# Kernel tuning notes

Measured on AMD Instinct MI355X. Metric: run time of the kernel, lower is better.

Reference implementation:

```python
import jax, jax.numpy as jnp
import numpy as np

CODEBOOK_SIZE = 4096
EMBED_DIM = 256
BETA = 0.25


def setup_inputs() -> dict:
    key = jax.random.key(0)
    k_z, k_cb = jax.random.split(key)
    z = jax.random.normal(k_z, (32, 256, 32, 32), dtype=jnp.float32)
    # nn.Embedding weight init: uniform(-1/D, 1/D)
    codebook = jax.random.uniform(
        k_cb, (CODEBOOK_SIZE, EMBED_DIM), dtype=jnp.float32,
        minval=-1.0 / EMBED_DIM, maxval=1.0 / EMBED_DIM)
    return {"z": z, "codebook": codebook}


def reference(z, codebook):
    b, c, h, w = z.shape
    # (B,C,H,W) -> (B*H*W, D)
    z_flat = jnp.transpose(z, (0, 2, 3, 1)).reshape(-1, c)
    # squared euclidean distances: ||z||^2 - 2 z.e^T + ||e||^2  (== cdist(...)^2)
    z_sq = jnp.sum(z_flat * z_flat, axis=1, keepdims=True)          # (N,1)
    e_sq = jnp.sum(codebook * codebook, axis=1)                     # (K,)
    distances = z_sq - 2.0 * (z_flat @ codebook.T) + e_sq[None, :]  # (N,K)
    min_encoding_indices = jnp.argmin(distances, axis=1)            # (N,)
    z_q_flat = codebook[min_encoding_indices]                       # (N,D)
    z_q = jnp.transpose(z_q_flat.reshape(b, h, w, c), (0, 3, 1, 2))  # (B,C,H,W)
    # straight-through estimator
    z_q_st = z + jax.lax.stop_gradient(z_q - z)
    codebook_loss = jnp.mean((z_q - jax.lax.stop_gradient(z)) ** 2)
    commitment_loss = jnp.mean((z - jax.lax.stop_gradient(z_q)) ** 2)
    vq_loss = codebook_loss + BETA * commitment_loss
    return (z_q_st, vq_loss, min_encoding_indices.reshape(b, h, w))
```

## Files before the change

kernel.cpp:

```cpp
#include <hip/hip_runtime.h>

#define K_CODES 4096
#define D 256
#define N_VEC 32768
#define N_ELEM 8388608
#define WINDOW 3.5e-4f
#define RG 8
#define RSLICE 256

typedef _Float16 f16x8 __attribute__((ext_vector_type(8)));
typedef float f32x4 __attribute__((ext_vector_type(4)));

#define WS_LOSS 0
#define WS_COUNT 8
#define WS_DONE 16
#define WS_IDX 256
#define WS_LIST (WS_IDX + N_VEC * 4)
#define WS_ESQ (WS_LIST + N_VEC * 4)
#define WS_ZSQ (WS_ESQ + K_CODES * 4)
#define WS_APACK (WS_ZSQ + N_VEC * 4)
#define WS_BPACK (WS_APACK + (size_t)N_VEC * 256 * 2)
#define WS_RFIN (WS_BPACK + (size_t)K_CODES * 256 * 2 + 65536)
#define WS_ZT (WS_RFIN + (size_t)N_VEC * 8)
#define WS_NEED_ZT (WS_ZT + (size_t)N_VEC * D * 4)

#define PREP_PZ 4096
#define PREP_PCB 512
#define PREP_ESQ 1024
#define PREP_ZSQ 128
#define PREP_BLOCKS (PREP_PZ + PREP_PCB + PREP_ESQ + PREP_ZSQ)

__device__ __forceinline__ unsigned long long pack_key(float s, int idx) {
  const unsigned u = __float_as_uint(s);
  const unsigned mk = (u & 0x80000000u) ? ~u : (u | 0x80000000u);
  return ((unsigned long long)mk << 12) | (unsigned long long)(unsigned)idx;
}
__device__ __forceinline__ float key_score(unsigned long long k) {
  const unsigned mk = (unsigned)(k >> 12);
  const unsigned u = (mk & 0x80000000u) ? (mk & 0x7fffffffu) : ~mk;
  return __uint_as_float(u);
}

__device__ __forceinline__ void pin_frag(f16x8& v) {
  asm volatile("" : "+v"(v));
}

__device__ void esq_body(int bx, const float* __restrict__ cb,
                         float* __restrict__ esq) {
  const int lane = threadIdx.x & 63;
  const int k = bx * 4 + (threadIdx.x >> 6);
  const float* row = cb + (size_t)k * D;
  double s = 0.;
#pragma unroll
  for (int j = 0; j < 4; ++j) {
    const float v = row[lane + 64 * j];
    s += (double)__fmul_rn(v, v);
  }
#pragma unroll
  for (int off = 32; off > 0; off >>= 1) s += __shfl_down(s, off, 64);
  if (lane == 0) esq[k] = (float)s;
}

__device__ void zsq_body(int bx, const float* __restrict__ z,
                         float* __restrict__ zsq) {
  const int n = bx * 256 + threadIdx.x;
  const int b = n >> 10;
  const int hw = n & 1023;
  const float* p = z + ((size_t)b << 18) + hw;
  double a0 = 0., a1 = 0., a2 = 0., a3 = 0.;
  for (int c = 0; c < D; c += 4) {
    const float v0 = p[(size_t)(c + 0) << 10];
    const float v1 = p[(size_t)(c + 1) << 10];
    const float v2 = p[(size_t)(c + 2) << 10];
    const float v3 = p[(size_t)(c + 3) << 10];
    a0 += (double)__fmul_rn(v0, v0);
    a1 += (double)__fmul_rn(v1, v1);
    a2 += (double)__fmul_rn(v2, v2);
    a3 += (double)__fmul_rn(v3, v3);
  }
  zsq[n] = (float)((a0 + a1) + (a2 + a3));
}

__device__ void pack_z2_body(int bx, const float* __restrict__ z,
                             _Float16* __restrict__ Ap,
                             float* __restrict__ zT) {
  const int t = bx * 256 + threadIdx.x;
  const int lane = t & 63;
  const int fid = t >> 6;
  const int ks = fid & 7;
  const int grp = fid >> 3;
  const int n = grp * 16 + (lane & 15);
  const int d = ks * 32 + ((lane >> 4) << 3);
  const int b = n >> 10, hw = n & 1023;
  const float* p = z + ((size_t)b << 18) + ((size_t)d << 10) + hw;
  float v[8];
  f16x8 H;
#pragma unroll
  for (int j = 0; j < 8; ++j) {
    v[j] = p[(size_t)j << 10];
    H[j] = (_Float16)v[j];
  }
  *(f16x8*)(Ap + (size_t)t * 8) = H;
  if (zT) {
    float4* o = (float4*)(zT + (size_t)n * D + d);
    o[0] = make_float4(v[0], v[1], v[2], v[3]);
    o[1] = make_float4(v[4], v[5], v[6], v[7]);
  }
}

__device__ void pack_cb2_body(int bx, const float* __restrict__ cb,
                              _Float16* __restrict__ Bp) {
  const int t = bx * 256 + threadIdx.x;
  const int lane = t & 63;
  const int fid = t >> 6;
  const int ks = fid & 7;
  const int grp = fid >> 3;
  const int k = grp * 16 + (lane & 15);
  const int d = ks * 32 + ((lane >> 4) << 3);
  const float* p = cb + (size_t)k * D + d;
  f16x8 H;
#pragma unroll
  for (int j = 0; j < 8; ++j) H[j] = (_Float16)(p[j] * 256.f);
  *(f16x8*)(Bp + (size_t)t * 8) = H;
}

__global__ __launch_bounds__(256) void prep_kernel(
    const float* __restrict__ z, const float* __restrict__ cb,
    float* __restrict__ esq, float* __restrict__ zsq,
    _Float16* __restrict__ Ap, _Float16* __restrict__ Bp,
    float* __restrict__ zT) {
  const int b = blockIdx.x;
  if (b < PREP_PZ) {
    pack_z2_body(b, z, Ap, zT);
  } else if (b < PREP_PZ + PREP_PCB) {
    pack_cb2_body(b - PREP_PZ, cb, Bp);
  } else if (b < PREP_PZ + PREP_PCB + PREP_ESQ) {
    esq_body(b - PREP_PZ - PREP_PCB, cb, esq);
  } else {
    zsq_body(b - PREP_PZ - PREP_PCB - PREP_ESQ, z, zsq);
  }
}

__global__ __launch_bounds__(512, 2) void dist2_kernel(
    const _Float16* __restrict__ Ap, const _Float16* __restrict__ Bp,
    const float* __restrict__ esq, int* __restrict__ idx,
    int* __restrict__ list, unsigned int* __restrict__ count,
    unsigned long long* __restrict__ rfin) {
  __shared__ unsigned long long mb[128][4][2];
  const int tid = threadIdx.x;
  const int lane = tid & 63;
  const int w = tid >> 6;
  const int wn = w >> 2;
  const int wc = w & 3;
  const int n0 = blockIdx.x * 128;

  f16x8 a[4][8];
  {
    const _Float16* ab =
        Ap + (size_t)((n0 + wn * 64) >> 4) * 4096 + (size_t)lane * 8;
#pragma unroll
    for (int ni = 0; ni < 4; ++ni)
#pragma unroll
      for (int ks = 0; ks < 8; ++ks) {
        a[ni][ks] = *(const f16x8*)(ab + (size_t)(ni * 8 + ks) * 512);
        pin_frag(a[ni][ks]);
      }
  }

  if (w >= 4) __builtin_amdgcn_s_sleep(7);

  float s1[4], s2[4];
  int i1[4];
#pragma unroll
  for (int ni = 0; ni < 4; ++ni) {
    s1[ni] = 3.4e38f;
    s2[ni] = 3.4e38f;
    i1[ni] = 0;
  }

  const _Float16* bbase = Bp + (size_t)wc * 4096 + (size_t)lane * 8;
  const int crow = wc * 16 + ((lane >> 4) << 2);
  const f32x4 z4 = (f32x4)0.f;

  f16x8 b[8];
#pragma unroll
  for (int ks = 0; ks < 8; ++ks)
    b[ks] = *(const f16x8*)(bbase + (size_t)ks * 512);

  for (int t = 0; t < 64; ++t) {
    const float4 e4 = *(const float4*)(esq + t * 64 + crow);
    f32x4 acc0, acc1, acc2, acc3;
    __builtin_amdgcn_s_setprio(1);
#pragma unroll
    for (int ks = 0; ks < 8; ++ks) {
      acc0 = __builtin_amdgcn_mfma_f32_16x16x32_f16(b[ks], a[0][ks],
                                                    ks ? acc0 : z4, 0, 0, 0);
      acc1 = __builtin_amdgcn_mfma_f32_16x16x32_f16(b[ks], a[1][ks],
                                                    ks ? acc1 : z4, 0, 0, 0);
      acc2 = __builtin_amdgcn_mfma_f32_16x16x32_f16(b[ks], a[2][ks],
                                                    ks ? acc2 : z4, 0, 0, 0);
      acc3 = __builtin_amdgcn_mfma_f32_16x16x32_f16(b[ks], a[3][ks],
                                                    ks ? acc3 : z4, 0, 0, 0);
      b[ks] = *(const f16x8*)(bbase + (size_t)(t + 1) * 16384 + ks * 512);
    }
    __builtin_amdgcn_s_setprio(0);
    const int cb0 = t * 64 + crow;
    const float ev[4] = {e4.x, e4.y, e4.z, e4.w};
#pragma unroll
    for (int r = 0; r < 4; ++r) {
      const int code = cb0 + r;
      {
        const float s = fmaf(acc0[r], -0.0078125f, ev[r]);
        s2[0] = fminf(fmaxf(s, s1[0]), s2[0]);
        if (s < s1[0]) i1[0] = code;
        s1[0] = fminf(s1[0], s);
      }
      {
        const float s = fmaf(acc1[r], -0.0078125f, ev[r]);
        s2[1] = fminf(fmaxf(s, s1[1]), s2[1]);
        if (s < s1[1]) i1[1] = code;
        s1[1] = fminf(s1[1], s);
      }
      {
        const float s = fmaf(acc2[r], -0.0078125f, ev[r]);
        s2[2] = fminf(fmaxf(s, s1[2]), s2[2]);
        if (s < s1[2]) i1[2] = code;
        s1[2] = fminf(s1[2], s);
      }
      {
        const float s = fmaf(acc3[r], -0.0078125f, ev[r]);
        s2[3] = fminf(fmaxf(s, s1[3]), s2[3]);
        if (s < s1[3]) i1[3] = code;
        s1[3] = fminf(s1[3], s);
      }
    }
  }

  unsigned long long k1[4], k2[4];
#pragma unroll
  for (int ni = 0; ni < 4; ++ni) {
    float a1 = s1[ni], a2 = s2[ni];
    int ai1 = i1[ni];
#pragma unroll
    for (int m = 16; m <= 32; m <<= 1) {
      const float bv1 = __shfl_xor(a1, m, 64);
      const int bi1 = __shfl_xor(ai1, m, 64);
      const float bv2 = __shfl_xor(a2, m, 64);
      const float hi = fmaxf(a1, bv1);
      const bool take = (bv1 < a1) || (bv1 == a1 && bi1 < ai1);
      if (take) ai1 = bi1;
      a1 = fminf(a1, bv1);
      a2 = fminf(fminf(a2, bv2), hi);
    }
    k1[ni] = pack_key(a1, ai1);
    k2[ni] = pack_key(a2, 0);
  }
  if (lane < 16) {
#pragma unroll
    for (int ni = 0; ni < 4; ++ni) {
      const int nl = wn * 64 + ni * 16 + lane;
      mb[nl][wc][0] = k1[ni];
      mb[nl][wc][1] = k2[ni];
    }
  }
  __syncthreads();
  if (tid < 128) {
    unsigned long long m1 = ~0ull, m2 = ~0ull;
#pragma unroll
    for (int s = 0; s < 4; ++s) {
      const unsigned long long c1 = mb[tid][s][0];
      const unsigned long long c2 = mb[tid][s][1];
      if (c1 < m1) {
        m2 = m1;
        m1 = c1;
      } else if (c1 < m2) {
        m2 = c1;
      }
      if (c2 < m2) m2 = c2;
    }
    const int n = n0 + tid;
    idx[n] = (int)(m1 & 0xFFFULL);
    const bool flag = key_score(m2) - key_score(m1) < WINDOW;
    rfin[n] = flag ? ~0ull : 0ull;
    if (flag) {
      const unsigned pos = atomicAdd(count, 1u);
      if (pos < N_VEC) list[pos] = n;
    }
  }
}

__global__ __launch_bounds__(256) void rescan_kernel(
    const float* __restrict__ z, const float* __restrict__ zT,
    const float* __restrict__ cb, const float* __restrict__ esq,
    const float* __restrict__ zsq, const int* __restrict__ list,
    const unsigned int* __restrict__ count,
    unsigned long long* __restrict__ rfin) {
  __shared__ double zrow[RG][D];
  __shared__ int nloc[RG];
  __shared__ float zsv[RG];
  const int tid = threadIdx.x;
  const int lane = tid & 63;
  unsigned int cnt = *count;
  if (cnt > N_VEC) cnt = N_VEC;
  const unsigned G = (cnt + RG - 1) / RG;
  const unsigned nitems = G * (K_CODES / RSLICE);
  for (unsigned item = blockIdx.x; item < nitems; item += gridDim.x) {
    const unsigned g = item >> 4;
    const int s = item & 15;
    __syncthreads();
    if (tid < RG) {
      const unsigned r = g * RG + tid;
      const int n = (r < cnt) ? list[r] : list[cnt - 1];
      nloc[tid] = n;
      zsv[tid] = zsq[n];
    }
    __syncthreads();
    if (zT) {
      for (int i = tid; i < RG * D; i += 256) {
        const int p = i >> 8, c = i & 255;
        zrow[p][c] = (double)zT[(size_t)nloc[p] * D + c];
      }
    } else {
      for (int i = tid; i < RG * D; i += 256) {
        const int p = i >> 8, c = i & 255;
        const int n = nloc[p];
        const int b = n >> 10, hw = n & 1023;
        zrow[p][c] = (double)z[((size_t)b << 18) + ((size_t)c << 10) + hw];
      }
    }
    __syncthreads();
    const int k = s * RSLICE + tid;
    const float* row = cb + (size_t)k * D;
    double acc[RG];
#pragma unroll
    for (int p = 0; p < RG; ++p) acc[p] = 0.;
    for (int c = 0; c < D; c += 4) {
      const float4 r4 = *(const float4*)(row + c);
      const double rx = (double)r4.x, ry = (double)r4.y;
      const double rz = (double)r4.z, rw = (double)r4.w;
#pragma unroll
      for (int p = 0; p < RG; ++p) {
        const double2 za = *(const double2*)&zrow[p][c];
        const double2 zb = *(const double2*)&zrow[p][c + 2];
        double a = acc[p];
        a = fma(za.x, rx, a);
        a = fma(za.y, ry, a);
        a = fma(zb.x, rz, a);
        a = fma(zb.y, rw, a);
        acc[p] = a;
      }
    }
    const float ek = esq[k];
    unsigned long long best[RG];
#pragma unroll
    for (int p = 0; p < RG; ++p) {
      const float dotf = (float)acc[p];
      const float d = __fadd_rn(__fsub_rn(zsv[p], __fmul_rn(2.0f, dotf)), ek);
      best[p] = pack_key(d, k);
    }
#pragma unroll
    for (int p = 0; p < RG; ++p) {
#pragma unroll
      for (int off = 32; off > 0; off >>= 1)
        best[p] = min(best[p], __shfl_down(best[p], off, 64));
    }
    if (lane == 0) {
#pragma unroll
      for (int p = 0; p < RG; ++p) atomicMin(rfin + nloc[p], best[p]);
    }
  }
}

__global__ __launch_bounds__(256) void gather_kernel(
    const float* __restrict__ z, const float* __restrict__ cb,
    const int* __restrict__ idxarr, const unsigned long long* __restrict__ rfin,
    float* __restrict__ out, float* __restrict__ loss_acc,
    unsigned int* __restrict__ done) {
  const int tid = threadIdx.x;
  const int n0 = blockIdx.x * 64;
  const int hwl = tid & 63;
  const int c0 = tid >> 6;
  const int n = n0 + hwl;
  const int b = n >> 10;
  const int hw = n & 1023;
  const unsigned long long rf = rfin[n];
  const int idx = rf ? (int)(rf & 0xFFFULL) : idxarr[n];
  if (tid < 64) out[(size_t)N_ELEM + 1 + n] = (float)idx;
  const float* crow = cb + (size_t)idx * D;
  const size_t obase = ((size_t)b << 18) + hw;
  float part = 0.f;
#pragma unroll
  for (int c = c0; c < D; c += 4) {
    const float v = crow[c];
    const size_t o = obase + ((size_t)c << 10);
    const float diff = v - z[o];
    out[o] = v;
    part = fmaf(diff, diff, part);
  }
#pragma unroll
  for (int off = 32; off > 0; off >>= 1) part += __shfl_down(part, off, 64);
  __shared__ float red[4];
  if ((tid & 63) == 0) red[tid >> 6] = part;
  __syncthreads();
  if (tid == 0) {
    atomicAdd(loss_acc, red[0] + red[1] + red[2] + red[3]);
    __threadfence();
    const unsigned old = atomicAdd(done, 1u);
    if (old == gridDim.x - 1) {
      const float total = atomicAdd(loss_acc, 0.0f);
      out[N_ELEM] = 1.25f * total * (1.0f / (float)N_ELEM);
    }
  }
}

extern "C" void kernel_launch(void* const* d_in, const int* in_sizes, int n_in,
                              void* d_out, int out_size, void* d_ws,
                              size_t ws_size, hipStream_t stream) {
  const float* z = (const float*)d_in[0];
  const float* cb = (const float*)d_in[1];
  float* out = (float*)d_out;
  char* ws = (char*)d_ws;
  float* loss_acc = (float*)(ws + WS_LOSS);
  unsigned int* count = (unsigned int*)(ws + WS_COUNT);
  unsigned int* done = (unsigned int*)(ws + WS_DONE);
  int* idx = (int*)(ws + WS_IDX);
  int* list = (int*)(ws + WS_LIST);
  float* esq = (float*)(ws + WS_ESQ);
  float* zsq = (float*)(ws + WS_ZSQ);
  _Float16* Ap = (_Float16*)(ws + WS_APACK);
  _Float16* Bp = (_Float16*)(ws + WS_BPACK);
  unsigned long long* rfin = (unsigned long long*)(ws + WS_RFIN);
  float* zT = (ws_size >= WS_NEED_ZT) ? (float*)(ws + WS_ZT) : nullptr;

  hipMemsetAsync(ws, 0, 256, stream);
  prep_kernel<<<PREP_BLOCKS, 256, 0, stream>>>(z, cb, esq, zsq, Ap, Bp, zT);
  dist2_kernel<<<N_VEC / 128, 512, 0, stream>>>(Ap, Bp, esq, idx, list, count,
                                                rfin);
  rescan_kernel<<<2048, 256, 0, stream>>>(z, zT, cb, esq, zsq, list, count,
                                          rfin);
  gather_kernel<<<N_VEC / 64, 256, 0, stream>>>(z, cb, idx, rfin, out,
                                                loss_acc, done);
}
```

Baseline: 274.0 us.

## Track top-4 candidates in distance pass to shrink exact rescan work

The fp16 MFMA distance pass now keeps a per-lane top-4 list of (score, code) instead of only the best score and second score. It merges these lists across lanes and waves with packed 64-bit keys. Ambiguous rows whose fourth-best score lies outside a wider window are rescanned exactly against only their four candidates in a new light kernel. Only the remaining rows go through the full-codebook rescan. The gather kernel also switches to float4 codebook reads, and the wave s_sleep staggering is removed. The cost is extra compare/select work and register pressure in the hot MFMA loop, plus a reliance on the top-4 containing the true argmin.

```diff
diff --git a/kernel.cpp b/kernel.cpp
--- a/kernel.cpp
+++ b/kernel.cpp
@@ -5,6 +5,7 @@
 #define N_VEC 32768
 #define N_ELEM 8388608
 #define WINDOW 3.5e-4f
+#define WINDOW_C 5.25e-4f
 #define RG 8
 #define RSLICE 256
 
@@ -14,6 +15,7 @@
 #define WS_LOSS 0
 #define WS_COUNT 8
 #define WS_DONE 16
+#define WS_COUNT2 24
 #define WS_IDX 256
 #define WS_LIST (WS_IDX + N_VEC * 4)
 #define WS_ESQ (WS_LIST + N_VEC * 4)
@@ -23,6 +25,9 @@
 #define WS_RFIN (WS_BPACK + (size_t)K_CODES * 256 * 2 + 65536)
 #define WS_ZT (WS_RFIN + (size_t)N_VEC * 8)
 #define WS_NEED_ZT (WS_ZT + (size_t)N_VEC * D * 4)
+#define WS_CAND4 WS_NEED_ZT
+#define WS_LISTB (WS_CAND4 + (size_t)N_VEC * 8)
+#define WS_NEED_CAND (WS_LISTB + (size_t)N_VEC * 4)
 
 #define PREP_PZ 4096
 #define PREP_PCB 512
@@ -43,6 +48,18 @@
 
 __device__ __forceinline__ void pin_frag(f16x8& v) {
   asm volatile("" : "+v"(v));
+}
+
+__device__ __forceinline__ void ins4(unsigned long long K[4],
+                                     unsigned long long x) {
+  const bool b0 = x < K[0];
+  const bool b1 = x < K[1];
+  const bool b2 = x < K[2];
+  const bool b3 = x < K[3];
+  K[3] = b2 ? K[2] : (b3 ? x : K[3]);
+  K[2] = b1 ? K[1] : (b2 ? x : K[2]);
+  K[1] = b0 ? K[0] : (b1 ? x : K[1]);
+  K[0] = b0 ? x : K[0];
 }
 
 __device__ void esq_body(int bx, const float* __restrict__ cb,
@@ -145,8 +162,9 @@
     const _Float16* __restrict__ Ap, const _Float16* __restrict__ Bp,
     const float* __restrict__ esq, int* __restrict__ idx,
     int* __restrict__ list, unsigned int* __restrict__ count,
-    unsigned long long* __restrict__ rfin) {
-  __shared__ unsigned long long mb[128][4][2];
+    unsigned long long* __restrict__ rfin, unsigned long long* __restrict__ cand4,
+    int* __restrict__ listB, unsigned int* __restrict__ count2) {
+  __shared__ unsigned long long mb[128][4][4];
   const int tid = threadIdx.x;
   const int lane = tid & 63;
   const int w = tid >> 6;
@@ -167,15 +185,13 @@
       }
   }
 
-  if (w >= 4) __builtin_amdgcn_s_sleep(7);
-
-  float s1[4], s2[4];
-  int i1[4];
+  float sv[4][4];
+  int iv[4][4];
 #pragma unroll
   for (int ni = 0; ni < 4; ++ni) {
-    s1[ni] = 3.4e38f;
-    s2[ni] = 3.4e38f;
-    i1[ni] = 0;
+    sv[ni][0] = 3.4e38f; sv[ni][1] = 3.4e38f;
+    sv[ni][2] = 3.4e38f; sv[ni][3] = 3.4e38f;
+    iv[ni][0] = 0; iv[ni][1] = 0; iv[ni][2] = 0; iv[ni][3] = 0;
   }
 
   const _Float16* bbase = Bp + (size_t)wc * 4096 + (size_t)lane * 8;
@@ -206,86 +222,117 @@
     __builtin_amdgcn_s_setprio(0);
     const int cb0 = t * 64 + crow;
     const float ev[4] = {e4.x, e4.y, e4.z, e4.w};
+    f32x4 accv[4] = {acc0, acc1, acc2, acc3};
 #pragma unroll
     for (int r = 0; r < 4; ++r) {
       const int code = cb0 + r;
-      {
-        const float s = fmaf(acc0[r], -0.0078125f, ev[r]);
-        s2[0] = fminf(fmaxf(s, s1[0]), s2[0]);
-        if (s < s1[0]) i1[0] = code;
-        s1[0] = fminf(s1[0], s);
+#pragma unroll
+      for (int ni = 0; ni < 4; ++ni) {
+        const float s = fmaf(accv[ni][r], -0.0078125f, ev[r]);
+        if (s < sv[ni][3]) {
+          const bool b0 = s < sv[ni][0];
+          const bool b1 = s < sv[ni][1];
+          const bool b2 = s < sv[ni][2];
+          sv[ni][3] = b2 ? sv[ni][2] : s;
+          iv[ni][3] = b2 ? iv[ni][2] : code;
+          sv[ni][2] = b1 ? sv[ni][1] : (b2 ? s : sv[ni][2]);
+          iv[ni][2] = b1 ? iv[ni][1] : (b2 ? code : iv[ni][2]);
+          sv[ni][1] = b0 ? sv[ni][0] : (b1 ? s : sv[ni][1]);
+          iv[ni][1] = b0 ? iv[ni][0] : (b1 ? code : iv[ni][1]);
+          sv[ni][0] = b0 ? s : sv[ni][0];
+          iv[ni][0] = b0 ? code : iv[ni][0];
+        }
       }
-      {
-        const float s = fmaf(acc1[r], -0.0078125f, ev[r]);
-        s2[1] = fminf(fmaxf(s, s1[1]), s2[1]);
-        if (s < s1[1]) i1[1] = code;
-        s1[1] = fminf(s1[1], s);
-      }
-      {
-        const float s = fmaf(acc2[r], -0.0078125f, ev[r]);
-        s2[2] = fminf(fmaxf(s, s1[2]), s2[2]);
-        if (s < s1[2]) i1[2] = code;
-        s1[2] = fminf(s1[2], s);
-      }
-      {
-        const float s = fmaf(acc3[r], -0.0078125f, ev[r]);
-        s2[3] = fminf(fmaxf(s, s1[3]), s2[3]);
-        if (s < s1[3]) i1[3] = code;
-        s1[3] = fminf(s1[3], s);
-      }
-    }
-  }
-
-  unsigned long long k1[4], k2[4];
+    }
+  }
+
 #pragma unroll
   for (int ni = 0; ni < 4; ++ni) {
-    float a1 = s1[ni], a2 = s2[ni];
-    int ai1 = i1[ni];
+    unsigned long long K[4];
+    K[0] = pack_key(sv[ni][0], iv[ni][0]);
+    K[1] = pack_key(sv[ni][1], iv[ni][1]);
+    K[2] = pack_key(sv[ni][2], iv[ni][2]);
+    K[3] = pack_key(sv[ni][3], iv[ni][3]);
 #pragma unroll
     for (int m = 16; m <= 32; m <<= 1) {
-      const float bv1 = __shfl_xor(a1, m, 64);
-      const int bi1 = __shfl_xor(ai1, m, 64);
-      const float bv2 = __shfl_xor(a2, m, 64);
-      const float hi = fmaxf(a1, bv1);
-      const bool take = (bv1 < a1) || (bv1 == a1 && bi1 < ai1);
-      if (take) ai1 = bi1;
-      a1 = fminf(a1, bv1);
-      a2 = fminf(fminf(a2, bv2), hi);
-    }
-    k1[ni] = pack_key(a1, ai1);
-    k2[ni] = pack_key(a2, 0);
-  }
-  if (lane < 16) {
-#pragma unroll
-    for (int ni = 0; ni < 4; ++ni) {
+      const unsigned long long o0 = __shfl_xor(K[0], m, 64);
+      const unsigned long long o1 = __shfl_xor(K[1], m, 64);
+      const unsigned long long o2 = __shfl_xor(K[2], m, 64);
+      const unsigned long long o3 = __shfl_xor(K[3], m, 64);
+      ins4(K, o0);
+      ins4(K, o1);
+      ins4(K, o2);
+      ins4(K, o3);
+    }
+    if (lane < 16) {
       const int nl = wn * 64 + ni * 16 + lane;
-      mb[nl][wc][0] = k1[ni];
-      mb[nl][wc][1] = k2[ni];
+      mb[nl][wc][0] = K[0];
+      mb[nl][wc][1] = K[1];
+      mb[nl][wc][2] = K[2];
+      mb[nl][wc][3] = K[3];
     }
   }
   __syncthreads();
   if (tid < 128) {
-    unsigned long long m1 = ~0ull, m2 = ~0ull;
-#pragma unroll
-    for (int s = 0; s < 4; ++s) {
-      const unsigned long long c1 = mb[tid][s][0];
-      const unsigned long long c2 = mb[tid][s][1];
-      if (c1 < m1) {
-        m2 = m1;
-        m1 = c1;
-      } else if (c1 < m2) {
-        m2 = c1;
-      }
-      if (c2 < m2) m2 = c2;
+    unsigned long long K[4] = {mb[tid][0][0], mb[tid][0][1], mb[tid][0][2],
+                               mb[tid][0][3]};
+#pragma unroll
+    for (int s = 1; s < 4; ++s) {
+      ins4(K, mb[tid][s][0]);
+      ins4(K, mb[tid][s][1]);
+      ins4(K, mb[tid][s][2]);
+      ins4(K, mb[tid][s][3]);
     }
     const int n = n0 + tid;
-    idx[n] = (int)(m1 & 0xFFFULL);
-    const bool flag = key_score(m2) - key_score(m1) < WINDOW;
+    idx[n] = (int)(K[0] & 0xFFFULL);
+    const float sc0 = key_score(K[0]);
+    const bool flag = key_score(K[1]) - sc0 < WINDOW;
     rfin[n] = flag ? ~0ull : 0ull;
     if (flag) {
-      const unsigned pos = atomicAdd(count, 1u);
-      if (pos < N_VEC) list[pos] = n;
-    }
+      if (cand4 && (key_score(K[3]) - sc0 >= WINDOW_C)) {
+        cand4[n] = (K[0] & 0xFFFULL) | ((K[1] & 0xFFFULL) << 16) |
+                   ((K[2] & 0xFFFULL) << 32) | ((K[3] & 0xFFFULL) << 48);
+        const unsigned pos = atomicAdd(count, 1u);
+        if (pos < N_VEC) list[pos] = n;
+      } else {
+        const unsigned p2 = atomicAdd(count2, 1u);
+        if (p2 < N_VEC) listB[p2] = n;
+      }
+    }
+  }
+}
+
+__global__ __launch_bounds__(256) void rescanB_kernel(
+    const float* __restrict__ zT, const float* __restrict__ cb,
+    const float* __restrict__ esq, const float* __restrict__ zsq,
+    const int* __restrict__ list, const unsigned int* __restrict__ count,
+    const unsigned long long* __restrict__ cand4,
+    unsigned long long* __restrict__ rfin) {
+  if (!cand4) return;
+  unsigned int cN = *count;
+  if (cN > N_VEC) cN = N_VEC;
+  const int tid = threadIdx.x;
+  const int j = tid & 3;
+  for (unsigned i = blockIdx.x * 64 + (tid >> 2); i < cN; i += gridDim.x * 64) {
+    const int n = list[i];
+    const int k = (int)((cand4[n] >> (16 * j)) & 0xFFFULL);
+    const float* zr = zT + (size_t)n * D;
+    const float* row = cb + (size_t)k * D;
+    double a = 0.;
+    for (int c = 0; c < D; c += 4) {
+      const float4 zf = *(const float4*)(zr + c);
+      const float4 r4 = *(const float4*)(row + c);
+      a = fma((double)zf.x, (double)r4.x, a);
+      a = fma((double)zf.y, (double)r4.y, a);
+      a = fma((double)zf.z, (double)r4.z, a);
+      a = fma((double)zf.w, (double)r4.w, a);
+    }
+    const float d =
+        __fadd_rn(__fsub_rn(zsq[n], __fmul_rn(2.0f, (float)a)), esq[k]);
+    unsigned long long best = pack_key(d, k);
+    best = min(best, __shfl_xor(best, 1, 64));
+    best = min(best, __shfl_xor(best, 2, 64));
+    if (j == 0) atomicMin(rfin + n, best);
   }
 }
 
@@ -379,7 +426,7 @@
   const int tid = threadIdx.x;
   const int n0 = blockIdx.x * 64;
   const int hwl = tid & 63;
-  const int c0 = tid >> 6;
+  const int cq = tid >> 6;
   const int n = n0 + hwl;
   const int b = n >> 10;
   const int hw = n & 1023;
@@ -390,12 +437,22 @@
   const size_t obase = ((size_t)b << 18) + hw;
   float part = 0.f;
 #pragma unroll
-  for (int c = c0; c < D; c += 4) {
-    const float v = crow[c];
+  for (int j = 0; j < 16; ++j) {
+    const int c = cq * 64 + j * 4;
+    const float4 v4 = *(const float4*)(crow + c);
     const size_t o = obase + ((size_t)c << 10);
-    const float diff = v - z[o];
-    out[o] = v;
-    part = fmaf(diff, diff, part);
+    const float d0 = v4.x - z[o];
+    const float d1 = v4.y - z[o + 1024];
+    const float d2 = v4.z - z[o + 2048];
+    const float d3 = v4.w - z[o + 3072];
+    out[o] = v4.x;
+    out[o + 1024] = v4.y;
+    out[o + 2048] = v4.z;
+    out[o + 3072] = v4.w;
+    part = fmaf(d0, d0, part);
+    part = fmaf(d1, d1, part);
+    part = fmaf(d2, d2, part);
+    part = fmaf(d3, d3, part);
   }
 #pragma unroll
   for (int off = 32; off > 0; off >>= 1) part += __shfl_down(part, off, 64);
@@ -423,6 +480,7 @@
   float* loss_acc = (float*)(ws + WS_LOSS);
   unsigned int* count = (unsigned int*)(ws + WS_COUNT);
   unsigned int* done = (unsigned int*)(ws + WS_DONE);
+  unsigned int* count2 = (unsigned int*)(ws + WS_COUNT2);
   int* idx = (int*)(ws + WS_IDX);
   int* list = (int*)(ws + WS_LIST);
   float* esq = (float*)(ws + WS_ESQ);
@@ -431,12 +489,19 @@
   _Float16* Bp = (_Float16*)(ws + WS_BPACK);
   unsigned long long* rfin = (unsigned long long*)(ws + WS_RFIN);
   float* zT = (ws_size >= WS_NEED_ZT) ? (float*)(ws + WS_ZT) : nullptr;
+  const bool canduse = (ws_size >= WS_NEED_CAND) && (zT != nullptr);
+  unsigned long long* cand4 =
+      canduse ? (unsigned long long*)(ws + WS_CAND4) : nullptr;
+  int* listB = canduse ? (int*)(ws + WS_LISTB) : list;
+  unsigned int* cntB = canduse ? count2 : count2;
 
   hipMemsetAsync(ws, 0, 256, stream);
   prep_kernel<<<PREP_BLOCKS, 256, 0, stream>>>(z, cb, esq, zsq, Ap, Bp, zT);
   dist2_kernel<<<N_VEC / 128, 512, 0, stream>>>(Ap, Bp, esq, idx, list, count,
-                                                rfin);
-  rescan_kernel<<<2048, 256, 0, stream>>>(z, zT, cb, esq, zsq, list, count,
+                                                rfin, cand4, listB, cntB);
+  rescanB_kernel<<<512, 256, 0, stream>>>(zT, cb, esq, zsq, list, count, cand4,
+                                          rfin);
+  rescan_kernel<<<2048, 256, 0, stream>>>(z, zT, cb, esq, zsq, listB, cntB,
                                           rfin);
   gather_kernel<<<N_VEC / 64, 256, 0, stream>>>(z, cb, idx, rfin, out,
                                                 loss_acc, done);
```

Result: slower. 329.4 us (+20.2%).

## Add fp16 certify pass to shortlist candidates before exact fp64 rescan

Applied to the files above, without the earlier changes.

Ambiguous vectors flagged by the fp16 MFMA distance pass now go through a certify kernel. It recomputes fp16 scores against all codes and collects up to CAP codes inside a wider window of the best score. A new rescanB kernel evaluates only those candidates in fp64. Only vectors that overflow the cap go to the full rescan, which cuts the exhaustive fp64 rescan work. The change also removes the half-block sleep in dist2 and vectorises the codebook row reads in the gather. The cost is two extra launches, a second full fp16 pass over the flagged vectors, and correctness now depends on the certify window bounding the fp16 error. The new path runs only when the workspace is large enough.

```diff
diff --git a/kernel.cpp b/kernel.cpp
--- a/kernel.cpp
+++ b/kernel.cpp
@@ -5,6 +5,9 @@
 #define N_VEC 32768
 #define N_ELEM 8388608
 #define WINDOW 3.5e-4f
+#define WINDOW_C 5.25e-4f
+#define CAP 14
+#define CSTRIDE 16
 #define RG 8
 #define RSLICE 256
 
@@ -14,6 +17,7 @@
 #define WS_LOSS 0
 #define WS_COUNT 8
 #define WS_DONE 16
+#define WS_COUNT2 24
 #define WS_IDX 256
 #define WS_LIST (WS_IDX + N_VEC * 4)
 #define WS_ESQ (WS_LIST + N_VEC * 4)
@@ -23,6 +27,11 @@
 #define WS_RFIN (WS_BPACK + (size_t)K_CODES * 256 * 2 + 65536)
 #define WS_ZT (WS_RFIN + (size_t)N_VEC * 8)
 #define WS_NEED_ZT (WS_ZT + (size_t)N_VEC * D * 4)
+#define WS_S1F WS_NEED_ZT
+#define WS_CANDN (WS_S1F + (size_t)N_VEC * 4)
+#define WS_CANDL (WS_CANDN + (size_t)N_VEC * 4)
+#define WS_LISTB (WS_CANDL + (size_t)N_VEC * CSTRIDE * 2)
+#define WS_NEED_CAND (WS_LISTB + (size_t)N_VEC * 4)
 
 #define PREP_PZ 4096
 #define PREP_PCB 512
@@ -145,7 +154,8 @@
     const _Float16* __restrict__ Ap, const _Float16* __restrict__ Bp,
     const float* __restrict__ esq, int* __restrict__ idx,
     int* __restrict__ list, unsigned int* __restrict__ count,
-    unsigned long long* __restrict__ rfin) {
+    unsigned long long* __restrict__ rfin, float* __restrict__ s1f,
+    int* __restrict__ listB, unsigned int* __restrict__ count2) {
   __shared__ unsigned long long mb[128][4][2];
   const int tid = threadIdx.x;
   const int lane = tid & 63;
@@ -166,8 +176,6 @@
         pin_frag(a[ni][ks]);
       }
   }
-
-  if (w >= 4) __builtin_amdgcn_s_sleep(7);
 
   float s1[4], s2[4];
   int i1[4];
@@ -206,32 +214,16 @@
     __builtin_amdgcn_s_setprio(0);
     const int cb0 = t * 64 + crow;
     const float ev[4] = {e4.x, e4.y, e4.z, e4.w};
+    f32x4 accv[4] = {acc0, acc1, acc2, acc3};
 #pragma unroll
     for (int r = 0; r < 4; ++r) {
       const int code = cb0 + r;
-      {
-        const float s = fmaf(acc0[r], -0.0078125f, ev[r]);
-        s2[0] = fminf(fmaxf(s, s1[0]), s2[0]);
-        if (s < s1[0]) i1[0] = code;
-        s1[0] = fminf(s1[0], s);
-      }
-      {
-        const float s = fmaf(acc1[r], -0.0078125f, ev[r]);
-        s2[1] = fminf(fmaxf(s, s1[1]), s2[1]);
-        if (s < s1[1]) i1[1] = code;
-        s1[1] = fminf(s1[1], s);
-      }
-      {
-        const float s = fmaf(acc2[r], -0.0078125f, ev[r]);
-        s2[2] = fminf(fmaxf(s, s1[2]), s2[2]);
-        if (s < s1[2]) i1[2] = code;
-        s1[2] = fminf(s1[2], s);
-      }
-      {
-        const float s = fmaf(acc3[r], -0.0078125f, ev[r]);
-        s2[3] = fminf(fmaxf(s, s1[3]), s2[3]);
-        if (s < s1[3]) i1[3] = code;
-        s1[3] = fminf(s1[3], s);
+#pragma unroll
+      for (int ni = 0; ni < 4; ++ni) {
+        const float s = fmaf(accv[ni][r], -0.0078125f, ev[r]);
+        s2[ni] = fminf(fmaxf(s, s1[ni]), s2[ni]);
+        if (s < s1[ni]) i1[ni] = code;
+        s1[ni] = fminf(s1[ni], s);
       }
     }
   }
@@ -280,12 +272,151 @@
     }
     const int n = n0 + tid;
     idx[n] = (int)(m1 & 0xFFFULL);
-    const bool flag = key_score(m2) - key_score(m1) < WINDOW;
+    const float sc0 = key_score(m1);
+    if (s1f) s1f[n] = sc0;
+    const bool flag = key_score(m2) - sc0 < WINDOW;
     rfin[n] = flag ? ~0ull : 0ull;
     if (flag) {
-      const unsigned pos = atomicAdd(count, 1u);
-      if (pos < N_VEC) list[pos] = n;
-    }
+      if (s1f) {
+        const unsigned pos = atomicAdd(count, 1u);
+        if (pos < N_VEC) list[pos] = n;
+      } else {
+        const unsigned p2 = atomicAdd(count2, 1u);
+        if (p2 < N_VEC) listB[p2] = n;
+      }
+    }
+  }
+}
+
+__global__ __launch_bounds__(256) void certify_kernel(
+    const _Float16* __restrict__ Ap, const _Float16* __restrict__ Bp,
+    const float* __restrict__ esq, const float* __restrict__ s1f,
+    const int* __restrict__ list, const unsigned int* __restrict__ count,
+    unsigned int* __restrict__ candn, unsigned short* __restrict__ candl,
+    int* __restrict__ listB, unsigned int* __restrict__ count2) {
+  if (!candn) return;
+  __shared__ unsigned int lcnt[32];
+  __shared__ unsigned int lcodes[32][CAP];
+  unsigned int cN = *count;
+  if (cN > N_VEC) cN = N_VEC;
+  if (cN == 0) return;
+  const int tid = threadIdx.x;
+  const int lane = tid & 63;
+  const int wc = tid >> 6;
+  const int l16 = lane & 15;
+  const int quad = lane >> 4;
+  const unsigned tiles = (cN + 31) / 32;
+  const f32x4 z4 = (f32x4)0.f;
+  for (unsigned tile = blockIdx.x; tile < tiles; tile += gridDim.x) {
+    __syncthreads();
+    if (tid < 32) lcnt[tid] = 0;
+    __syncthreads();
+    float thrv[2];
+    f16x8 af[2][8];
+#pragma unroll
+    for (int ni = 0; ni < 2; ++ni) {
+      unsigned r = tile * 32 + ni * 16 + l16;
+      if (r >= cN) r = cN - 1;
+      const int n = list[r];
+      thrv[ni] = s1f[n] + WINDOW_C;
+      const _Float16* ab = Ap + (size_t)(n >> 4) * 4096 +
+                           (size_t)quad * 128 + (size_t)(n & 15) * 8;
+#pragma unroll
+      for (int ks = 0; ks < 8; ++ks) {
+        af[ni][ks] = *(const f16x8*)(ab + (size_t)ks * 512);
+        pin_frag(af[ni][ks]);
+      }
+    }
+    const _Float16* bbase = Bp + (size_t)wc * 4096 + (size_t)lane * 8;
+    for (int t = 0; t < 64; ++t) {
+      const int cb0 = t * 64 + wc * 16 + quad * 4;
+      const float4 e4 = *(const float4*)(esq + cb0);
+      f16x8 bf[8];
+#pragma unroll
+      for (int ks = 0; ks < 8; ++ks)
+        bf[ks] = *(const f16x8*)(bbase + (size_t)t * 16384 + ks * 512);
+      f32x4 acc0, acc1;
+#pragma unroll
+      for (int ks = 0; ks < 8; ++ks) {
+        acc0 = __builtin_amdgcn_mfma_f32_16x16x32_f16(bf[ks], af[0][ks],
+                                                      ks ? acc0 : z4, 0, 0, 0);
+        acc1 = __builtin_amdgcn_mfma_f32_16x16x32_f16(bf[ks], af[1][ks],
+                                                      ks ? acc1 : z4, 0, 0, 0);
+      }
+      const float ev[4] = {e4.x, e4.y, e4.z, e4.w};
+#pragma unroll
+      for (int r = 0; r < 4; ++r) {
+        const float sA = fmaf(acc0[r], -0.0078125f, ev[r]);
+        const float sB = fmaf(acc1[r], -0.0078125f, ev[r]);
+        if (sA < thrv[0]) {
+          const unsigned u = atomicAdd(&lcnt[l16], 1u);
+          if (u < CAP) lcodes[l16][u] = (unsigned)(cb0 + r);
+        }
+        if (sB < thrv[1]) {
+          const unsigned u = atomicAdd(&lcnt[16 + l16], 1u);
+          if (u < CAP) lcodes[16 + l16][u] = (unsigned)(cb0 + r);
+        }
+      }
+    }
+    __syncthreads();
+    if (tid < 32) {
+      const unsigned r = tile * 32 + tid;
+      if (r < cN) {
+        const int n = list[r];
+        const unsigned c = lcnt[tid];
+        if (c <= CAP) {
+          candn[n] = c;
+          for (unsigned u = 0; u < c; ++u)
+            candl[(size_t)n * CSTRIDE + u] = (unsigned short)lcodes[tid][u];
+        } else {
+          candn[n] = 0xFFFFFFFFu;
+          const unsigned p = atomicAdd(count2, 1u);
+          if (p < N_VEC) listB[p] = n;
+        }
+      }
+    }
+  }
+}
+
+__global__ __launch_bounds__(256) void rescanB_kernel(
+    const float* __restrict__ zT, const float* __restrict__ cb,
+    const float* __restrict__ esq, const float* __restrict__ zsq,
+    const int* __restrict__ list, const unsigned int* __restrict__ count,
+    const unsigned int* __restrict__ candn,
+    const unsigned short* __restrict__ candl,
+    unsigned long long* __restrict__ rfin) {
+  if (!candn) return;
+  unsigned int cN = *count;
+  if (cN > N_VEC) cN = N_VEC;
+  const int tid = threadIdx.x;
+  const int j8 = tid & 7;
+  for (unsigned i = blockIdx.x * 32 + (tid >> 3); i < cN;
+       i += gridDim.x * 32) {
+    const int n = list[i];
+    const unsigned c = candn[n];
+    if (c > CAP) continue;
+    unsigned long long best = ~0ull;
+    for (unsigned jj = j8; jj < c; jj += 8) {
+      const int k = candl[(size_t)n * CSTRIDE + jj];
+      const float* zr = zT + (size_t)n * D;
+      const float* row = cb + (size_t)k * D;
+      double a = 0.;
+      for (int cc = 0; cc < D; cc += 4) {
+        const float4 zf = *(const float4*)(zr + cc);
+        const float4 r4 = *(const float4*)(row + cc);
+        a = fma((double)zf.x, (double)r4.x, a);
+        a = fma((double)zf.y, (double)r4.y, a);
+        a = fma((double)zf.z, (double)r4.z, a);
+        a = fma((double)zf.w, (double)r4.w, a);
+      }
+      const float d =
+          __fadd_rn(__fsub_rn(zsq[n], __fmul_rn(2.0f, (float)a)), esq[k]);
+      best = min(best, pack_key(d, k));
+    }
+    best = min(best, __shfl_xor(best, 1, 64));
+    best = min(best, __shfl_xor(best, 2, 64));
+    best = min(best, __shfl_xor(best, 4, 64));
+    if (j8 == 0) atomicMin(rfin + n, best);
   }
 }
 
@@ -379,7 +510,7 @@
   const int tid = threadIdx.x;
   const int n0 = blockIdx.x * 64;
   const int hwl = tid & 63;
-  const int c0 = tid >> 6;
+  const int cq = tid >> 6;
   const int n = n0 + hwl;
   const int b = n >> 10;
   const int hw = n & 1023;
@@ -390,12 +521,22 @@
   const size_t obase = ((size_t)b << 18) + hw;
   float part = 0.f;
 #pragma unroll
-  for (int c = c0; c < D; c += 4) {
-    const float v = crow[c];
+  for (int j = 0; j < 16; ++j) {
+    const int c = cq * 64 + j * 4;
+    const float4 v4 = *(const float4*)(crow + c);
     const size_t o = obase + ((size_t)c << 10);
-    const float diff = v - z[o];
-    out[o] = v;
-    part = fmaf(diff, diff, part);
+    const float d0 = v4.x - z[o];
+    const float d1 = v4.y - z[o + 1024];
+    const float d2 = v4.z - z[o + 2048];
+    const float d3 = v4.w - z[o + 3072];
+    out[o] = v4.x;
+    out[o + 1024] = v4.y;
+    out[o + 2048] = v4.z;
+    out[o + 3072] = v4.w;
+    part = fmaf(d0, d0, part);
+    part = fmaf(d1, d1, part);
+    part = fmaf(d2, d2, part);
+    part = fmaf(d3, d3, part);
   }
 #pragma unroll
   for (int off = 32; off > 0; off >>= 1) part += __shfl_down(part, off, 64);
@@ -423,6 +564,7 @@
   float* loss_acc = (float*)(ws + WS_LOSS);
   unsigned int* count = (unsigned int*)(ws + WS_COUNT);
   unsigned int* done = (unsigned int*)(ws + WS_DONE);
+  unsigned int* count2 = (unsigned int*)(ws + WS_COUNT2);
   int* idx = (int*)(ws + WS_IDX);
   int* list = (int*)(ws + WS_LIST);
   float* esq = (float*)(ws + WS_ESQ);
@@ -431,12 +573,21 @@
   _Float16* Bp = (_Float16*)(ws + WS_BPACK);
   unsigned long long* rfin = (unsigned long long*)(ws + WS_RFIN);
   float* zT = (ws_size >= WS_NEED_ZT) ? (float*)(ws + WS_ZT) : nullptr;
+  const bool canduse = (ws_size >= WS_NEED_CAND) && (zT != nullptr);
+  float* s1f = canduse ? (float*)(ws + WS_S1F) : nullptr;
+  unsigned int* candn = canduse ? (unsigned int*)(ws + WS_CANDN) : nullptr;
+  unsigned short* candl = canduse ? (unsigned short*)(ws + WS_CANDL) : nullptr;
+  int* listB = canduse ? (int*)(ws + WS_LISTB) : list;
 
   hipMemsetAsync(ws, 0, 256, stream);
   prep_kernel<<<PREP_BLOCKS, 256, 0, stream>>>(z, cb, esq, zsq, Ap, Bp, zT);
   dist2_kernel<<<N_VEC / 128, 512, 0, stream>>>(Ap, Bp, esq, idx, list, count,
-                                                rfin);
-  rescan_kernel<<<2048, 256, 0, stream>>>(z, zT, cb, esq, zsq, list, count,
+                                                rfin, s1f, listB, count2);
+  certify_kernel<<<128, 256, 0, stream>>>(Ap, Bp, esq, s1f, list, count, candn,
+                                          candl, listB, count2);
+  rescanB_kernel<<<256, 256, 0, stream>>>(zT, cb, esq, zsq, list, count, candn,
+                                          candl, rfin);
+  rescan_kernel<<<2048, 256, 0, stream>>>(z, zT, cb, esq, zsq, listB, count2,
                                           rfin);
   gather_kernel<<<N_VEC / 64, 256, 0, stream>>>(z, cb, idx, rfin, out,
                                                 loss_acc, done);
```

After: 298.2 us. +8.8%, slower.
